# Kernel optimization log

Measured on AMD Instinct MI355X. Metric: run time of the kernel, lower is better.

## Reference

```python
import jax, jax.numpy as jnp
import numpy as np

LN_EPS = 1e-6


def setup_inputs() -> dict:
    key = jax.random.key(0)
    ks = jax.random.split(key, 8)
    B, L, D = 8, 4096, 1024
    s = 1.0 / np.sqrt(D)
    inputs = jax.random.normal(ks[0], (B, L, D), dtype=jnp.float32)
    # PositionwiseFeedForward params (d_ff == d_model here)
    w1 = jax.random.normal(ks[1], (D, D), dtype=jnp.float32) * s
    b1 = jnp.zeros((D,), dtype=jnp.float32)
    w2 = jax.random.normal(ks[2], (D, D), dtype=jnp.float32) * s
    b2 = jnp.zeros((D,), dtype=jnp.float32)
    ln_g = jnp.ones((D,), dtype=jnp.float32)
    ln_b = jnp.zeros((D,), dtype=jnp.float32)
    # gating layer: Linear(2D, 2D)
    wg = jax.random.normal(ks[3], (2 * D, 2 * D), dtype=jnp.float32) * (1.0 / np.sqrt(2 * D))
    bg = jnp.zeros((2 * D,), dtype=jnp.float32)
    return {"inputs": inputs, "w1": w1, "b1": b1, "w2": w2, "b2": b2,
            "ln_g": ln_g, "ln_b": ln_b, "wg": wg, "bg": bg}


def _layer_norm(x, g, b):
    mu = jnp.mean(x, axis=-1, keepdims=True)
    var = jnp.mean(jnp.square(x - mu), axis=-1, keepdims=True)
    return (x - mu) * jax.lax.rsqrt(var + LN_EPS) * g + b


def reference(inputs, w1, b1, w2, b2, ln_g, ln_b, wg, bg):
    B, L, D = inputs.shape
    # Cumulative average: identical math to tril(ones)/arange mask @ inputs,
    # computed in O(L) via prefix sum instead of an O(L^2) matmul.
    denom = jnp.arange(1, L + 1, dtype=inputs.dtype)[:, None]  # [L,1]
    avg = jnp.cumsum(inputs, axis=1) / denom                    # [B,L,D]
    # PositionwiseFeedForward (eval mode, dropout=0): LN -> relu(Linear) -> Linear -> +residual
    h = _layer_norm(avg, ln_g, ln_b)
    inter = jax.nn.relu(jnp.einsum('bld,df->blf', h, w1) + b1)
    avg_out = jnp.einsum('blf,fd->bld', inter, w2) + b2 + avg
    # Gating: Linear on concat(inputs, avg_out), split, sigmoid gates
    concat = jnp.concatenate([inputs, avg_out], axis=-1)        # [B,L,2D]
    gates = jnp.einsum('ble,ef->blf', concat, wg) + bg          # [B,L,2D]
    input_gate, forget_gate = gates[..., :D], gates[..., D:]
    out = jax.nn.sigmoid(input_gate) * inputs + jax.nn.sigmoid(forget_gate) * avg_out
    return out
```

## Files before the change

kernel.cpp:

```cpp
#include <hip/hip_runtime.h>

typedef __bf16 bf16_t;
typedef bf16_t bf16x8 __attribute__((ext_vector_type(8)));
typedef bf16_t bf16x4 __attribute__((ext_vector_type(4)));
typedef float  f32x4  __attribute__((ext_vector_type(4)));

typedef const __attribute__((address_space(1))) void* gptr_t;
typedef __attribute__((address_space(3))) void* sptr_t;

#define BATCH 8
#define SEQL  4096
#define DIM   1024
#define MROWS 32768

__device__ __forceinline__ float sigmoidf_(float v) {
    return 1.0f / (1.0f + __expf(-v));
}

template <int PERM>
__global__ void transpose_cast(const float* __restrict__ W, bf16_t* __restrict__ WT,
                               int K, int N) {
    __shared__ float s[32][33];
    int tx = threadIdx.x, ty = threadIdx.y;
    int x = blockIdx.x * 32 + tx;
    int y = blockIdx.y * 32 + ty;
    s[ty][tx] = W[(size_t)y * N + x];
    __syncthreads();
    int n = blockIdx.x * 32 + ty;
    int k = blockIdx.y * 32 + tx;
    int nd = n;
    if (PERM) {
        if (n < 1024) nd = ((n >> 6) << 7) + (n & 63);
        else          nd = (((n - 1024) >> 6) << 7) + 64 + ((n - 1024) & 63);
    }
    WT[(size_t)nd * K + k] = (bf16_t)s[tx][ty];
}

__global__ void scan_chunks(const float* __restrict__ x, float* __restrict__ cs) {
    int tid = threadIdx.x;
    int b = blockIdx.x >> 6, c = blockIdx.x & 63;
    const f32x4* x4 = (const f32x4*)x;
    size_t base = ((size_t)b * SEQL + (size_t)c * 64) * 256 + tid;
    f32x4 s0 = {0.f, 0.f, 0.f, 0.f}, s1 = {0.f, 0.f, 0.f, 0.f};
#pragma unroll 8
    for (int j = 0; j < 64; j += 2) {
        s0 += x4[base + (size_t)j * 256];
        s1 += x4[base + (size_t)(j + 1) * 256];
    }
    ((f32x4*)cs)[((size_t)(b << 6) + c) * 256 + tid] = s0 + s1;
}

__global__ void scan_prefix(float* __restrict__ cs) {
    int t = blockIdx.x * 256 + threadIdx.x;
    int b = t >> 10, d = t & 1023;
    size_t base = (size_t)(b << 6) * 1024 + d;
    float v[64];
#pragma unroll
    for (int c = 0; c < 64; ++c) v[c] = cs[base + (size_t)c * 1024];
    float run = 0.f;
#pragma unroll
    for (int c = 0; c < 64; ++c) {
        float tv = v[c];
        cs[base + (size_t)c * 1024] = run;
        run += tv;
    }
}

__global__ __launch_bounds__(256) void scan_ln(
    const float* __restrict__ x, const float* __restrict__ cs,
    const float* __restrict__ g, const float* __restrict__ bb,
    float* __restrict__ avg, bf16_t* __restrict__ hb, bf16_t* __restrict__ xb) {
    int tid = threadIdx.x;
    int wave = tid >> 6, lane = tid & 63;
    int b = blockIdx.x >> 6, c = blockIdx.x & 63;
    __shared__ float red[8];
    const f32x4* x4 = (const f32x4*)x;
    f32x4* avg4 = (f32x4*)avg;
    bf16x4* hb4 = (bf16x4*)hb;
    bf16x4* xb4 = (bf16x4*)xb;
    f32x4 run = ((const f32x4*)cs)[((size_t)(b << 6) + c) * 256 + tid];
    f32x4 gv = ((const f32x4*)g)[tid];
    f32x4 bv = ((const f32x4*)bb)[tid];
    size_t row0 = (size_t)b * SEQL + (size_t)c * 64;
    f32x4 xv = x4[row0 * 256 + tid];
    for (int j = 0; j < 64; ++j) {
        size_t ridx = (row0 + j) * 256 + tid;
        f32x4 xnext = {0.f, 0.f, 0.f, 0.f};
        if (j < 63) xnext = x4[ridx + 256];
        run += xv;
        float inv = 1.0f / (float)(c * 64 + j + 1);
        f32x4 av = run * inv;
        avg4[ridx] = av;
        bf16x4 xo = { (bf16_t)xv[0], (bf16_t)xv[1], (bf16_t)xv[2], (bf16_t)xv[3] };
        xb4[ridx] = xo;
        float s  = av[0] + av[1] + av[2] + av[3];
        float sq = av[0]*av[0] + av[1]*av[1] + av[2]*av[2] + av[3]*av[3];
#pragma unroll
        for (int off = 32; off; off >>= 1) {
            s  += __shfl_xor(s, off);
            sq += __shfl_xor(sq, off);
        }
        if (lane == 0) { red[wave] = s; red[4 + wave] = sq; }
        __syncthreads();
        s  = red[0] + red[1] + red[2] + red[3];
        sq = red[4] + red[5] + red[6] + red[7];
        float mu  = s * (1.f / DIM);
        float var = sq * (1.f / DIM) - mu * mu;
        var = var < 0.f ? 0.f : var;
        float rs = 1.0f / sqrtf(var + 1e-6f);
        f32x4 hn = (av - mu) * rs * gv + bv;
        bf16x4 ho = { (bf16_t)hn[0], (bf16_t)hn[1], (bf16_t)hn[2], (bf16_t)hn[3] };
        hb4[ridx] = ho;
        __syncthreads();
        xv = xnext;
    }
}

template <int EPI>
__global__ __launch_bounds__(512, 2) void gemm_bt(
    const bf16_t* __restrict__ A0, const bf16_t* __restrict__ A1, int kSplit,
    const bf16_t* __restrict__ Bt, int N, int K,
    const float* __restrict__ bias, const float* __restrict__ addsrc,
    const float* __restrict__ xsrc,
    float* __restrict__ outf, bf16_t* __restrict__ outb) {
    __shared__ char smem[131072];
    const int tid = threadIdx.x;
    const int wave = tid >> 6, lane = tid & 63;

    const int nwg = gridDim.x;
    const int q8 = nwg >> 3;
    const int lid = (blockIdx.x & 7) * q8 + ((int)blockIdx.x >> 3);
    const int nBlocks = N >> 8;
    const int m0 = (lid / nBlocks) << 8;
    const int n0 = (lid % nBlocks) << 8;

    const int wm = (wave >> 2) << 7;
    const int wn = (wave & 3) << 6;
    const int lrow16 = lane & 15;
    const int ksw0 = ((((lane >> 4) + 0) ^ (lane & 7)) << 3);
    const int ksw1 = ((((lane >> 4) + 4) ^ (lane & 7)) << 3);

    f32x4 acc[8][4] = {};

    auto stageA = [&](int kt, int buf, int mh) {
        const int k0 = kt << 6;
        const bf16_t* Asrc; int ak0;
        if (k0 < kSplit) { Asrc = A0; ak0 = k0; }
        else             { Asrc = A1; ak0 = k0 - kSplit; }
#pragma unroll
        for (int rr = 0; rr < 2; ++rr) {
            int ci = tid + ((mh + rr * 2) << 9);
            int row = ci >> 3, ch = ci & 7;
            int chs = ch ^ (row & 7);
            const bf16_t* gp = Asrc + (size_t)(m0 + row) * kSplit + ak0 + (chs << 3);
            bf16_t* sb = (bf16_t*)(smem + (buf << 16)) + (size_t)(ci & ~63) * 8;
            __builtin_amdgcn_global_load_lds((gptr_t)gp, (sptr_t)sb, 16, 0, 0);
        }
    };
    auto stageB = [&](int kt, int buf, int half) {
        const int k0 = kt << 6;
#pragma unroll
        for (int rr = 0; rr < 2; ++rr) {
            int ci = tid + ((half * 2 + rr) << 9);
            int row = ci >> 3, ch = ci & 7;
            int chs = ch ^ (row & 7);
            const bf16_t* gp = Bt + (size_t)(n0 + row) * K + k0 + (chs << 3);
            bf16_t* sb = (bf16_t*)(smem + (buf << 16) + 32768) + (size_t)(ci & ~63) * 8;
            __builtin_amdgcn_global_load_lds((gptr_t)gp, (sptr_t)sb, 16, 0, 0);
        }
    };

    bf16x8 af[4], bfv0[4], bfv1[4];
    auto readsAB = [&](int buf, int mh, int ksw, bf16x8* bfv) {
        const bf16_t* As_ = (const bf16_t*)(smem + (buf << 16));
        const bf16_t* Bs_ = As_ + 16384;
#pragma unroll
        for (int ni = 0; ni < 4; ++ni)
            bfv[ni] = *(const bf16x8*)&Bs_[(wn + ni * 16 + lrow16) * 64 + ksw];
#pragma unroll
        for (int mi = 0; mi < 4; ++mi)
            af[mi] = *(const bf16x8*)&As_[(wm + (mh * 4 + mi) * 16 + lrow16) * 64 + ksw];
    };
    auto readsA = [&](int buf, int mh, int ksw) {
        const bf16_t* As_ = (const bf16_t*)(smem + (buf << 16));
#pragma unroll
        for (int mi = 0; mi < 4; ++mi)
            af[mi] = *(const bf16x8*)&As_[(wm + (mh * 4 + mi) * 16 + lrow16) * 64 + ksw];
    };
    auto mfma16 = [&](int mh, bf16x8* bfv) {
        __builtin_amdgcn_s_setprio(1);
#pragma unroll
        for (int mi = 0; mi < 4; ++mi)
#pragma unroll
            for (int ni = 0; ni < 4; ++ni)
                acc[mh * 4 + mi][ni] = __builtin_amdgcn_mfma_f32_16x16x32_bf16(
                    af[mi], bfv[ni], acc[mh * 4 + mi][ni], 0, 0, 0);
        __builtin_amdgcn_s_setprio(0);
    };

#define BAR_  __builtin_amdgcn_s_barrier()
#define SB_   __builtin_amdgcn_sched_barrier(0)
#define VMW6_ asm volatile("s_waitcnt vmcnt(6)" ::: "memory")

    stageA(0, 0, 0);
    stageB(0, 0, 0);
    stageB(0, 0, 1);
    stageA(1, 1, 0);
    stageA(0, 0, 1);

    const int nIter = K >> 7;
#pragma nounroll
    for (int i = 0; i < nIter; ++i) {
        const int t2 = i << 1;
        stageB(t2 + 1, 1, 0);
        VMW6_; BAR_; SB_;
        readsAB(0, 0, ksw0, bfv0); mfma16(0, bfv0);
        SB_; BAR_; SB_;

        stageB(t2 + 1, 1, 1);
        BAR_; SB_;
        readsAB(0, 0, ksw1, bfv1); mfma16(0, bfv1);
        SB_; BAR_; SB_;

        stageA(t2 + 2, 0, 0);
        VMW6_; BAR_; SB_;
        readsA(0, 1, ksw0); mfma16(1, bfv0);
        SB_; BAR_; SB_;

        stageA(t2 + 1, 1, 1);
        BAR_; SB_;
        readsA(0, 1, ksw1); mfma16(1, bfv1);
        SB_; BAR_; SB_;

        stageB(t2 + 2, 0, 0);
        VMW6_; BAR_; SB_;
        readsAB(1, 0, ksw0, bfv0); mfma16(0, bfv0);
        SB_; BAR_; SB_;

        stageB(t2 + 2, 0, 1);
        BAR_; SB_;
        readsAB(1, 0, ksw1, bfv1); mfma16(0, bfv1);
        SB_; BAR_; SB_;

        stageA(t2 + 3, 1, 0);
        VMW6_; BAR_; SB_;
        readsA(1, 1, ksw0); mfma16(1, bfv0);
        SB_; BAR_; SB_;

        stageA(t2 + 2, 0, 1);
        BAR_; SB_;
        readsA(1, 1, ksw1); mfma16(1, bfv1);
        SB_; BAR_; SB_;
    }
    asm volatile("s_waitcnt vmcnt(0)" ::: "memory");

#undef BAR_
#undef SB_
#undef VMW6_

    const int erow = (lane >> 4) << 2;

    if (EPI == 4) {
        __syncthreads();
        float* xch = (float*)smem;
        const int T = (n0 + wn) >> 7;
        const int pairOff = ((((wave >> 2) << 1) | ((wave >> 1) & 1))) << 13;
        if (wn & 64) {
#pragma unroll
            for (int mi = 0; mi < 8; ++mi) {
#pragma unroll
                for (int ni = 0; ni < 4; ++ni) {
                    int dc = ni * 16 + lrow16;
                    float bcol = bias[1024 + T * 64 + dc];
                    int d = T * 64 + dc;
#pragma unroll
                    for (int r = 0; r < 4; ++r) {
                        int rowW = mi * 16 + erow + r;
                        int row = m0 + wm + rowW;
                        float v = acc[mi][ni][r] + bcol;
                        int sw = ((rowW >> 2) & 1) << 4;
                        xch[pairOff + rowW * 64 + (dc ^ sw)] =
                            sigmoidf_(v) * addsrc[(size_t)row * 1024 + d];
                    }
                }
            }
        }
        __syncthreads();
        if (!(wn & 64)) {
#pragma unroll
            for (int mi = 0; mi < 8; ++mi) {
#pragma unroll
                for (int ni = 0; ni < 4; ++ni) {
                    int dc = ni * 16 + lrow16;
                    float bcol = bias[T * 64 + dc];
                    int d = T * 64 + dc;
#pragma unroll
                    for (int r = 0; r < 4; ++r) {
                        int rowW = mi * 16 + erow + r;
                        int row = m0 + wm + rowW;
                        float v = acc[mi][ni][r] + bcol;
                        int sw = ((rowW >> 2) & 1) << 4;
                        float tot = sigmoidf_(v) * xsrc[(size_t)row * 1024 + d]
                                  + xch[pairOff + rowW * 64 + (dc ^ sw)];
                        outf[(size_t)row * 1024 + d] = tot;
                    }
                }
            }
        }
        return;
    }

#pragma unroll
    for (int mi = 0; mi < 8; ++mi) {
#pragma unroll
        for (int ni = 0; ni < 4; ++ni) {
            int col = n0 + wn + ni * 16 + lrow16;
            float bcol = bias[col];
#pragma unroll
            for (int r = 0; r < 4; ++r) {
                int row = m0 + wm + mi * 16 + erow + r;
                size_t idx = (size_t)row * N + col;
                float v = acc[mi][ni][r];
                if (EPI == 1) {
                    v += bcol;
                    v = v > 0.f ? v : 0.f;
                    outb[idx] = (bf16_t)v;
                } else {
                    v += bcol + addsrc[idx];
                    outf[idx] = v;
                    outb[idx] = (bf16_t)v;
                }
            }
        }
    }
}

extern "C" void kernel_launch(void* const* d_in, const int* in_sizes, int n_in,
                              void* d_out, int out_size, void* d_ws, size_t ws_size,
                              hipStream_t stream) {
    const float* inp  = (const float*)d_in[0];
    const float* w1   = (const float*)d_in[1];
    const float* b1   = (const float*)d_in[2];
    const float* w2   = (const float*)d_in[3];
    const float* b2   = (const float*)d_in[4];
    const float* ln_g = (const float*)d_in[5];
    const float* ln_b = (const float*)d_in[6];
    const float* wg   = (const float*)d_in[7];
    const float* bg   = (const float*)d_in[8];
    float* out = (float*)d_out;

    char* w = (char*)d_ws;
    float*  avg    = (float*)w;   w += (size_t)MROWS * DIM * 4;
    float*  avgout = (float*)w;   w += (size_t)MROWS * DIM * 4;
    bf16_t* xb     = (bf16_t*)w;  w += (size_t)MROWS * DIM * 2;
    bf16_t* hb     = (bf16_t*)w;  w += (size_t)MROWS * DIM * 2;
    bf16_t* interb = (bf16_t*)w;  w += (size_t)MROWS * DIM * 2;
    bf16_t* w1t    = (bf16_t*)w;  w += (size_t)DIM * DIM * 2;
    bf16_t* w2t    = (bf16_t*)w;  w += (size_t)DIM * DIM * 2;
    bf16_t* wgt    = (bf16_t*)w;  w += (size_t)2 * DIM * 2 * DIM * 2;
    float*  csum   = (float*)w;   w += (size_t)BATCH * 64 * DIM * 4;
    bf16_t* aob    = hb;

    transpose_cast<0><<<dim3(32, 32), dim3(32, 32), 0, stream>>>(w1, w1t, DIM, DIM);
    transpose_cast<0><<<dim3(32, 32), dim3(32, 32), 0, stream>>>(w2, w2t, DIM, DIM);
    transpose_cast<1><<<dim3(64, 64), dim3(32, 32), 0, stream>>>(wg, wgt, 2 * DIM, 2 * DIM);

    scan_chunks<<<BATCH * 64, 256, 0, stream>>>(inp, csum);
    scan_prefix<<<32, 256, 0, stream>>>(csum);
    scan_ln<<<BATCH * 64, 256, 0, stream>>>(inp, csum, ln_g, ln_b, avg, hb, xb);

    gemm_bt<1><<<(MROWS / 256) * (DIM / 256), 512, 0, stream>>>(
        hb, hb, DIM, w1t, DIM, DIM, b1, nullptr, nullptr, nullptr, interb);

    gemm_bt<2><<<(MROWS / 256) * (DIM / 256), 512, 0, stream>>>(
        interb, interb, DIM, w2t, DIM, DIM, b2, avg, nullptr, avgout, aob);

    gemm_bt<4><<<(MROWS / 256) * (2 * DIM / 256), 512, 0, stream>>>(
        xb, aob, DIM, wgt, 2 * DIM, 2 * DIM, bg, avgout, inp, out, nullptr);
}
```

Before: 878.6 us.

## Triple-buffer B tiles and restructure GEMM main loop prefetch schedule

```diff
diff --git a/kernel.cpp b/kernel.cpp
--- a/kernel.cpp
+++ b/kernel.cpp
@@ -123,7 +123,7 @@
     const float* __restrict__ bias, const float* __restrict__ addsrc,
     const float* __restrict__ xsrc,
     float* __restrict__ outf, bf16_t* __restrict__ outb) {
-    __shared__ char smem[131072];
+    __shared__ char smem[163840];
     const int tid = threadIdx.x;
     const int wave = tid >> 6, lane = tid & 63;
 
@@ -142,50 +142,48 @@
 
     f32x4 acc[8][4] = {};
 
-    auto stageA = [&](int kt, int buf, int mh) {
+    auto stageA = [&](int kt, int mh) {
         const int k0 = kt << 6;
         const bf16_t* Asrc; int ak0;
         if (k0 < kSplit) { Asrc = A0; ak0 = k0; }
         else             { Asrc = A1; ak0 = k0 - kSplit; }
+        char* base = smem + ((kt & 1) << 15);
 #pragma unroll
         for (int rr = 0; rr < 2; ++rr) {
             int ci = tid + ((mh + rr * 2) << 9);
             int row = ci >> 3, ch = ci & 7;
             int chs = ch ^ (row & 7);
             const bf16_t* gp = Asrc + (size_t)(m0 + row) * kSplit + ak0 + (chs << 3);
-            bf16_t* sb = (bf16_t*)(smem + (buf << 16)) + (size_t)(ci & ~63) * 8;
+            bf16_t* sb = (bf16_t*)base + (size_t)(ci & ~63) * 8;
             __builtin_amdgcn_global_load_lds((gptr_t)gp, (sptr_t)sb, 16, 0, 0);
         }
     };
-    auto stageB = [&](int kt, int buf, int half) {
+    auto stageB = [&](int kt, int slot, int half) {
         const int k0 = kt << 6;
+        char* base = smem + 65536 + (slot << 15);
 #pragma unroll
         for (int rr = 0; rr < 2; ++rr) {
             int ci = tid + ((half * 2 + rr) << 9);
             int row = ci >> 3, ch = ci & 7;
             int chs = ch ^ (row & 7);
             const bf16_t* gp = Bt + (size_t)(n0 + row) * K + k0 + (chs << 3);
-            bf16_t* sb = (bf16_t*)(smem + (buf << 16) + 32768) + (size_t)(ci & ~63) * 8;
+            bf16_t* sb = (bf16_t*)base + (size_t)(ci & ~63) * 8;
             __builtin_amdgcn_global_load_lds((gptr_t)gp, (sptr_t)sb, 16, 0, 0);
         }
     };
 
     bf16x8 af[4], bfv0[4], bfv1[4];
-    auto readsAB = [&](int buf, int mh, int ksw, bf16x8* bfv) {
-        const bf16_t* As_ = (const bf16_t*)(smem + (buf << 16));
-        const bf16_t* Bs_ = As_ + 16384;
+    auto readA = [&](int buf, int mh, int ksw) {
+        const bf16_t* As_ = (const bf16_t*)(smem + (buf << 15));
+#pragma unroll
+        for (int mi = 0; mi < 4; ++mi)
+            af[mi] = *(const bf16x8*)&As_[(wm + (mh * 4 + mi) * 16 + lrow16) * 64 + ksw];
+    };
+    auto readB = [&](int slot, int ksw, bf16x8* bfv) {
+        const bf16_t* Bs_ = (const bf16_t*)(smem + 65536 + (slot << 15));
 #pragma unroll
         for (int ni = 0; ni < 4; ++ni)
             bfv[ni] = *(const bf16x8*)&Bs_[(wn + ni * 16 + lrow16) * 64 + ksw];
-#pragma unroll
-        for (int mi = 0; mi < 4; ++mi)
-            af[mi] = *(const bf16x8*)&As_[(wm + (mh * 4 + mi) * 16 + lrow16) * 64 + ksw];
-    };
-    auto readsA = [&](int buf, int mh, int ksw) {
-        const bf16_t* As_ = (const bf16_t*)(smem + (buf << 16));
-#pragma unroll
-        for (int mi = 0; mi < 4; ++mi)
-            af[mi] = *(const bf16x8*)&As_[(wm + (mh * 4 + mi) * 16 + lrow16) * 64 + ksw];
     };
     auto mfma16 = [&](int mh, bf16x8* bfv) {
         __builtin_amdgcn_s_setprio(1);
@@ -200,62 +198,68 @@
 
 #define BAR_  __builtin_amdgcn_s_barrier()
 #define SB_   __builtin_amdgcn_sched_barrier(0)
+#define LG0_  asm volatile("s_waitcnt lgkmcnt(0)" ::: "memory")
 #define VMW6_ asm volatile("s_waitcnt vmcnt(6)" ::: "memory")
 
-    stageA(0, 0, 0);
+    stageA(0, 0);
+    stageA(0, 1);
     stageB(0, 0, 0);
     stageB(0, 0, 1);
-    stageA(1, 1, 0);
-    stageA(0, 0, 1);
+    stageA(1, 0);
+    stageB(1, 1, 0);
+    stageB(1, 1, 1);
+    VMW6_;
+    BAR_;
 
     const int nIter = K >> 7;
+    int sA = 0;
 #pragma nounroll
     for (int i = 0; i < nIter; ++i) {
-        const int t2 = i << 1;
-        stageB(t2 + 1, 1, 0);
-        VMW6_; BAR_; SB_;
-        readsAB(0, 0, ksw0, bfv0); mfma16(0, bfv0);
-        SB_; BAR_; SB_;
-
-        stageB(t2 + 1, 1, 1);
-        BAR_; SB_;
-        readsAB(0, 0, ksw1, bfv1); mfma16(0, bfv1);
-        SB_; BAR_; SB_;
-
-        stageA(t2 + 2, 0, 0);
-        VMW6_; BAR_; SB_;
-        readsA(0, 1, ksw0); mfma16(1, bfv0);
-        SB_; BAR_; SB_;
-
-        stageA(t2 + 1, 1, 1);
-        BAR_; SB_;
-        readsA(0, 1, ksw1); mfma16(1, bfv1);
-        SB_; BAR_; SB_;
-
-        stageB(t2 + 2, 0, 0);
-        VMW6_; BAR_; SB_;
-        readsAB(1, 0, ksw0, bfv0); mfma16(0, bfv0);
-        SB_; BAR_; SB_;
-
-        stageB(t2 + 2, 0, 1);
-        BAR_; SB_;
-        readsAB(1, 0, ksw1, bfv1); mfma16(0, bfv1);
-        SB_; BAR_; SB_;
-
-        stageA(t2 + 3, 1, 0);
-        VMW6_; BAR_; SB_;
-        readsA(1, 1, ksw0); mfma16(1, bfv0);
-        SB_; BAR_; SB_;
-
-        stageA(t2 + 2, 0, 1);
-        BAR_; SB_;
-        readsA(1, 1, ksw1); mfma16(1, bfv1);
-        SB_; BAR_; SB_;
+        const int t0 = i << 1;
+        int sl1 = sA + 1; if (sl1 >= 3) sl1 -= 3;
+        int sl2 = sl1 + 1; if (sl2 >= 3) sl2 -= 3;
+
+        readA(0, 0, ksw0); readB(sA, ksw0, bfv0);
+        stageA(t0 + 1, 1);
+        BAR_; LG0_; SB_; mfma16(0, bfv0); BAR_;
+
+        readA(0, 0, ksw1); readB(sA, ksw1, bfv1);
+        stageB(t0 + 2, sl2, 0);
+        BAR_; LG0_; SB_; mfma16(0, bfv1); BAR_;
+
+        readA(0, 1, ksw0);
+        stageA(t0 + 2, 0);
+        BAR_; LG0_; SB_; mfma16(1, bfv0); BAR_;
+
+        readA(0, 1, ksw1);
+        stageB(t0 + 2, sl2, 1);
+        VMW6_;
+        BAR_; LG0_; SB_; mfma16(1, bfv1); BAR_;
+
+        readA(1, 0, ksw0); readB(sl1, ksw0, bfv0);
+        stageA(t0 + 2, 1);
+        BAR_; LG0_; SB_; mfma16(0, bfv0); BAR_;
+
+        readA(1, 0, ksw1); readB(sl1, ksw1, bfv1);
+        stageB(t0 + 3, sA, 0);
+        BAR_; LG0_; SB_; mfma16(0, bfv1); BAR_;
+
+        readA(1, 1, ksw0);
+        stageA(t0 + 3, 0);
+        BAR_; LG0_; SB_; mfma16(1, bfv0); BAR_;
+
+        readA(1, 1, ksw1);
+        stageB(t0 + 3, sA, 1);
+        VMW6_;
+        BAR_; LG0_; SB_; mfma16(1, bfv1); BAR_;
+
+        sA += 2; if (sA >= 3) sA -= 3;
     }
     asm volatile("s_waitcnt vmcnt(0)" ::: "memory");
 
 #undef BAR_
 #undef SB_
+#undef LG0_
 #undef VMW6_
 
     const int erow = (lane >> 4) << 2;
```

Measured after the change: 873.2 us. No clear change (-0.6%).
